# Kernel tuning notes

Measured on AMD Instinct MI355X. Metric: run time of the kernel, lower is better.

The kernel has to match this reference:

```python
import jax, jax.numpy as jnp
import numpy as np

B = 1024          # batch
IN_FEATURES = 20000
N_GROUP = 64
G_IN = 512        # indices gathered per group
H1 = 256          # first Linear out dim per group
GROUP_SIZE = 128  # second Linear out dim per group


def setup_inputs() -> dict:
    key = jax.random.key(0)
    k_x, k_idx, k_w1, k_b1, k_w2, k_b2 = jax.random.split(key, 6)
    x = jax.random.normal(k_x, (B, IN_FEATURES), dtype=jnp.float32)
    idx = jax.random.randint(k_idx, (N_GROUP, G_IN), 0, IN_FEATURES, dtype=jnp.int64)
    # Stacked per-group Linear weights (uniform group shapes allow batching).
    s1 = 1.0 / np.sqrt(G_IN)
    s2 = 1.0 / np.sqrt(H1)
    W1 = jax.random.uniform(k_w1, (N_GROUP, G_IN, H1), jnp.float32, -s1, s1)
    b1 = jax.random.uniform(k_b1, (N_GROUP, H1), jnp.float32, -s1, s1)
    W2 = jax.random.uniform(k_w2, (N_GROUP, H1, GROUP_SIZE), jnp.float32, -s2, s2)
    b2 = jax.random.uniform(k_b2, (N_GROUP, GROUP_SIZE), jnp.float32, -s2, s2)
    return {"x": x, "idx": idx, "W1": W1, "b1": b1, "W2": W2, "b2": b2}


def reference(x, idx, W1, b1, W2, b2):
    # Per-group gather of input columns: [B, n_group, G_IN]
    g = x[:, idx]
    # Two bare Linears per group (no activation, matching the source Sequential).
    h = jnp.einsum('bgi,gio->bgo', g, W1) + b1          # [B, n_group, H1]
    o = jnp.einsum('bgh,gho->bgo', h, W2) + b2          # [B, n_group, GROUP_SIZE]
    # Concat groups along feature dim -> [B, n_group*GROUP_SIZE]
    return o.reshape(o.shape[0], -1)
```

## Files before the change

kernel.cpp:

```cpp
#include <hip/hip_runtime.h>
#include <hip/hip_bf16.h>
#include <stdint.h>


typedef __attribute__((ext_vector_type(4))) float f32x4;
typedef __attribute__((ext_vector_type(8))) __bf16 bf16x8;
typedef __attribute__((ext_vector_type(8))) uint16_t u16x8;

__device__ __forceinline__ uint16_t f2bf(float f) {
    uint32_t u = __float_as_uint(f);
    u += 0x7FFFu + ((u >> 16) & 1u);
    return (uint16_t)(u >> 16);
}

__device__ __forceinline__ uint64_t pack4bf(f32x4 v) {
    return (uint64_t)f2bf(v[0]) | ((uint64_t)f2bf(v[1]) << 16)
         | ((uint64_t)f2bf(v[2]) << 32) | ((uint64_t)f2bf(v[3]) << 48);
}

__device__ __forceinline__ uint32_t bf16lo(float f) {
    uint32_t q;
    asm("v_cvt_pk_bf16_f32 %0, %1, 0" : "=v"(q) : "v"(f));
    return q;
}

__global__ __launch_bounds__(1024, 8) void k_prep(const float* __restrict__ x,
                                                  const int* __restrict__ idx,
                                                  const float* __restrict__ W1,
                                                  const float* __restrict__ b1,
                                                  const float* __restrict__ W2,
                                                  const float* __restrict__ b2,
                                                  uint16_t* __restrict__ Wc,
                                                  float* __restrict__ bias2,
                                                  uint32_t* __restrict__ G32) {
    __shared__ __align__(16) uint8_t smem[81920];
    const int bid = blockIdx.x;
    const int t = threadIdx.x;

    if (bid < 256) {
        uint16_t* As = (uint16_t*)smem;
        uint16_t* Bs = As + 5120;
        const int g = bid >> 2, mt = bid & 3;
        const int wid = t >> 6, l = t & 63;
        const int wm = wid >> 2, wn = wid & 3;
        const int q = l >> 4, lm = l & 15;
        const float* W1g = W1 + ((size_t)g * 512 + (size_t)mt * 128) * 256;
        const float* W2g = W2 + (size_t)g * 256 * 128;
        f32x4 acc[2][2];
        #pragma unroll
        for (int mi = 0; mi < 2; ++mi)
            #pragma unroll
            for (int ni = 0; ni < 2; ++ni) {
                f32x4 z = {0.f, 0.f, 0.f, 0.f};
                acc[mi][ni] = z;
            }
        for (int kt = 0; kt < 8; ++kt) {
            __syncthreads();
            {
                int m = t >> 3, c4 = t & 7;
                f32x4 v = *(const f32x4*)(W1g + (size_t)m * 256 + kt * 32 + c4 * 4);
                *(uint64_t*)&As[m * 40 + c4 * 4] = pack4bf(v);
            }
            {
                int h = t >> 5, n4 = t & 31;
                f32x4 v = *(const f32x4*)(W2g + (size_t)(kt * 32 + h) * 128 + n4 * 4);
                *(uint64_t*)&Bs[h * 132 + n4 * 4] = pack4bf(v);
            }
            __syncthreads();
            bf16x8 a[2];
            #pragma unroll
            for (int mi = 0; mi < 2; ++mi)
                a[mi] = *(const bf16x8*)&As[(wm * 32 + mi * 16 + lm) * 40 + q * 8];
            #pragma unroll
            for (int ni = 0; ni < 2; ++ni) {
                int n = wn * 32 + ni * 16 + lm;
                u16x8 bu;
                #pragma unroll
                for (int j = 0; j < 8; ++j) bu[j] = Bs[(q * 8 + j) * 132 + n];
                bf16x8 bv = __builtin_bit_cast(bf16x8, bu);
                #pragma unroll
                for (int mi = 0; mi < 2; ++mi)
                    acc[mi][ni] = __builtin_amdgcn_mfma_f32_16x16x32_bf16(a[mi], bv, acc[mi][ni], 0, 0, 0);
            }
        }
        uint16_t* Wcg = Wc + (size_t)g * 128 * 512;
        #pragma unroll
        for (int mi = 0; mi < 2; ++mi) {
            int k0 = mt * 128 + wm * 32 + mi * 16 + q * 4;
            #pragma unroll
            for (int ni = 0; ni < 2; ++ni) {
                int n = wn * 32 + ni * 16 + lm;
                *(uint64_t*)&Wcg[(size_t)n * 512 + k0] = pack4bf(acc[mi][ni]);
            }
        }
    } else if (bid < 320) {
        if (t < 128) {
            const int g = bid - 256, n = t;
            const float* w = W2 + (size_t)g * 256 * 128 + n;
            const float* bb = b1 + g * 256;
            float s = b2[g * 128 + n];
            for (int h = 0; h < 256; ++h) s += bb[h] * w[(size_t)h * 128];
            bias2[g * 128 + n] = s;
        }
    } else {
        uint32_t* sh32 = (uint32_t*)smem;
        const int gb = bid - 320;
        const int b0 = gb * 2, b1r = b0 + 1;
        const float* xr0 = x + (size_t)b0 * 20000;
        const float* xr1 = xr0 + 20000;

        f32x4 r0[5], r1[5];
        #pragma unroll
        for (int i = 0; i < 5; ++i) {
            int c = t + i * 1024;
            int cs = c < 5000 ? c : 4999;
            r0[i] = *(const f32x4*)(xr0 + (size_t)cs * 4);
        }
        #pragma unroll
        for (int i = 0; i < 5; ++i) {
            int c = t + i * 1024;
            int cs = c < 5000 ? c : 4999;
            r1[i] = *(const f32x4*)(xr1 + (size_t)cs * 4);
        }
        #pragma unroll
        for (int i = 0; i < 5; ++i) {
            int c = t + i * 1024;
            uint4 qv;
            qv.x = bf16lo(r0[i][0]);
            qv.y = bf16lo(r0[i][1]);
            qv.z = bf16lo(r0[i][2]);
            qv.w = bf16lo(r0[i][3]);
            *(uint4*)&sh32[c * 4] = qv;
        }
        #pragma unroll
        for (int i = 0; i < 5; ++i) {
            int c = t + i * 1024;
            uint16_t* hp = (uint16_t*)&sh32[c * 4];
            #pragma unroll
            for (int j = 0; j < 4; ++j)
                hp[j * 2 + 1] = (uint16_t)bf16lo(r1[i][j]);
        }
        __syncthreads();

        const int4* idx4 = (const int4*)idx;
        uint32_t* rowA = G32 + (size_t)b0 * 16384;
        uint32_t* rowB = G32 + (size_t)b1r * 16384;
        #pragma unroll
        for (int it = 0; it < 4; ++it) {
            int j8 = t + it * 1024;
            int4 va = idx4[j8 * 2];
            int4 vb = idx4[j8 * 2 + 1];
            uint32_t f0 = sh32[va.x], f1 = sh32[va.y];
            uint32_t f2 = sh32[va.z], f3 = sh32[va.w];
            uint32_t f4 = sh32[vb.x], f5 = sh32[vb.y];
            uint32_t f6 = sh32[vb.z], f7 = sh32[vb.w];
            uint4 p0, p1;
            p0.x = __builtin_amdgcn_perm(f1, f0, 0x05040100u);
            p0.y = __builtin_amdgcn_perm(f3, f2, 0x05040100u);
            p0.z = __builtin_amdgcn_perm(f5, f4, 0x05040100u);
            p0.w = __builtin_amdgcn_perm(f7, f6, 0x05040100u);
            p1.x = __builtin_amdgcn_perm(f1, f0, 0x07060302u);
            p1.y = __builtin_amdgcn_perm(f3, f2, 0x07060302u);
            p1.z = __builtin_amdgcn_perm(f5, f4, 0x07060302u);
            p1.w = __builtin_amdgcn_perm(f7, f6, 0x07060302u);
            *(uint4*)&rowA[j8 * 4] = p0;
            *(uint4*)&rowB[j8 * 4] = p1;
        }
    }
}

__global__ __launch_bounds__(256) void k_gemm(const uint16_t* __restrict__ G,
                                              const uint16_t* __restrict__ Wc,
                                              const float* __restrict__ bias2,
                                              float* __restrict__ out) {
    __shared__ uint16_t sh[12288];
    uint16_t* As = sh;
    uint16_t* Bs = sh + 4096;
    const int wg = (blockIdx.x & 7) * 128 + (blockIdx.x >> 3);
    const int g = wg >> 4, mt = wg & 15;
    const int t = threadIdx.x;
    const int wid = t >> 6, l = t & 63;
    const int wm = wid >> 1, wn = wid & 1;
    const int q = l >> 4, lm = l & 15;
    const int lrow = l >> 3;
    const int lcolsw = ((l & 7) ^ lrow) * 8;
    const uint16_t* Ga = G + (size_t)mt * 64 * 32768 + (size_t)g * 512;
    const uint16_t* Wa = Wc + (size_t)g * 65536;

    f32x4 acc[2][4];
    #pragma unroll
    for (int mi = 0; mi < 2; ++mi)
        #pragma unroll
        for (int ni = 0; ni < 4; ++ni) {
            f32x4 z = {0.f, 0.f, 0.f, 0.f};
            acc[mi][ni] = z;
        }

    for (int kt = 0; kt < 8; ++kt) {
        __syncthreads();
        #pragma unroll
        for (int i = 0; i < 2; ++i) {
            const int rowbase = wid * 8 + i * 32;
            const uint16_t* sA = Ga + (size_t)(rowbase + lrow) * 32768 + kt * 64 + lcolsw;
            __builtin_amdgcn_global_load_lds(
                (const __attribute__((address_space(1))) void*)sA,
                (__attribute__((address_space(3))) void*)(As + rowbase * 64), 16, 0, 0);
        }
        #pragma unroll
        for (int i = 0; i < 4; ++i) {
            const int rowbase = wid * 8 + i * 32;
            const uint16_t* sB = Wa + (size_t)(rowbase + lrow) * 512 + kt * 64 + lcolsw;
            __builtin_amdgcn_global_load_lds(
                (const __attribute__((address_space(1))) void*)sB,
                (__attribute__((address_space(3))) void*)(Bs + rowbase * 64), 16, 0, 0);
        }
        __syncthreads();
        #pragma unroll
        for (int kk = 0; kk < 2; ++kk) {
            bf16x8 a[2], b[4];
            #pragma unroll
            for (int mi = 0; mi < 2; ++mi) {
                int row = wm * 32 + mi * 16 + lm;
                int off = row * 64 + ((kk * 32 + q * 8) ^ ((lm & 7) * 8));
                a[mi] = *(const bf16x8*)&As[off];
            }
            #pragma unroll
            for (int ni = 0; ni < 4; ++ni) {
                int row = wn * 64 + ni * 16 + lm;
                int off = row * 64 + ((kk * 32 + q * 8) ^ ((lm & 7) * 8));
                b[ni] = *(const bf16x8*)&Bs[off];
            }
            #pragma unroll
            for (int mi = 0; mi < 2; ++mi)
                #pragma unroll
                for (int ni = 0; ni < 4; ++ni)
                    acc[mi][ni] = __builtin_amdgcn_mfma_f32_16x16x32_bf16(a[mi], b[ni], acc[mi][ni], 0, 0, 0);
        }
    }
    float bn[4];
    #pragma unroll
    for (int ni = 0; ni < 4; ++ni) bn[ni] = bias2[g * 128 + wn * 64 + ni * 16 + lm];
    #pragma unroll
    for (int mi = 0; mi < 2; ++mi)
        #pragma unroll
        for (int ni = 0; ni < 4; ++ni) {
            int col = g * 128 + wn * 64 + ni * 16 + lm;
            #pragma unroll
            for (int r = 0; r < 4; ++r) {
                int brow = mt * 64 + wm * 32 + mi * 16 + q * 4 + r;
                out[(size_t)brow * 8192 + col] = acc[mi][ni][r] + bn[ni];
            }
        }
}

extern "C" void kernel_launch(void* const* d_in, const int* in_sizes, int n_in,
                              void* d_out, int out_size, void* d_ws, size_t ws_size,
                              hipStream_t stream) {
    (void)in_sizes; (void)n_in; (void)out_size; (void)ws_size;
    const float* x   = (const float*)d_in[0];
    const int*   idx = (const int*)d_in[1];
    const float* W1  = (const float*)d_in[2];
    const float* b1  = (const float*)d_in[3];
    const float* W2  = (const float*)d_in[4];
    const float* b2  = (const float*)d_in[5];
    float* out = (float*)d_out;

    uint16_t* G     = (uint16_t*)d_ws;
    uint16_t* Wc    = (uint16_t*)((char*)d_ws + (size_t)(64 << 20));
    float*    bias2 = (float*)   ((char*)d_ws + (size_t)(72 << 20));

    k_prep<<<832, 1024, 0, stream>>>(x, idx, W1, b1, W2, b2, Wc, bias2, (uint32_t*)G);
    k_gemm<<<1024, 256, 0, stream>>>(G, Wc, bias2, out);
}
```

Baseline: 57.60 us.

## Split gather blocks into two staged rows with separate bf16 buffers

Gather blocks used to load two x rows, interleave them as packed bf16 pairs in one LDS array, and emit both output rows with permute ops. Now each row is staged alone into its own 16-bit LDS buffer using a paired bf16 convert, then gathered, so the second row's loads can overlap the first row's gather. Row order alternates with block parity, which may spread memory traffic. In exchange the gather now does 16-bit LDS reads and shift/or packing, there are two barriers, and fewer registers hold loaded data at once.

```diff
diff --git a/kernel.cpp b/kernel.cpp
--- a/kernel.cpp
+++ b/kernel.cpp
@@ -18,10 +18,41 @@
          | ((uint64_t)f2bf(v[2]) << 32) | ((uint64_t)f2bf(v[3]) << 48);
 }
 
-__device__ __forceinline__ uint32_t bf16lo(float f) {
-    uint32_t q;
-    asm("v_cvt_pk_bf16_f32 %0, %1, 0" : "=v"(q) : "v"(f));
-    return q;
+__device__ __forceinline__ void stage_row(uint16_t* buf, const float* __restrict__ xrow,
+                                          int t) {
+    #pragma unroll
+    for (int i = 0; i < 5; ++i) {
+        int c = t + i * 1024;
+        int cs = c < 5000 ? c : 4999;
+        f32x4 v = *(const f32x4*)(xrow + (size_t)cs * 4);
+        uint32_t lo, hi;
+        asm("v_cvt_pk_bf16_f32 %0, %1, %2" : "=v"(lo) : "v"(v[0]), "v"(v[1]));
+        asm("v_cvt_pk_bf16_f32 %0, %1, %2" : "=v"(hi) : "v"(v[2]), "v"(v[3]));
+        uint2 p2; p2.x = lo; p2.y = hi;
+        *(uint2*)&buf[c * 4] = p2;
+    }
+}
+
+__device__ __forceinline__ void gather_row(const uint16_t* buf, const int* __restrict__ idx,
+                                           int t, int b, uint32_t* __restrict__ G32) {
+    const int4* idx4 = (const int4*)idx;
+    uint32_t* row = G32 + (size_t)b * 16384;
+    #pragma unroll
+    for (int it = 0; it < 4; ++it) {
+        int j8 = t + it * 1024;
+        int4 va = idx4[j8 * 2];
+        int4 vb = idx4[j8 * 2 + 1];
+        uint32_t f0 = buf[va.x], f1 = buf[va.y];
+        uint32_t f2 = buf[va.z], f3 = buf[va.w];
+        uint32_t f4 = buf[vb.x], f5 = buf[vb.y];
+        uint32_t f6 = buf[vb.z], f7 = buf[vb.w];
+        uint4 p;
+        p.x = f0 | (f1 << 16);
+        p.y = f2 | (f3 << 16);
+        p.z = f4 | (f5 << 16);
+        p.w = f6 | (f7 << 16);
+        *(uint4*)&row[j8 * 4] = p;
+    }
 }
 
 __global__ __launch_bounds__(1024, 8) void k_prep(const float* __restrict__ x,
@@ -103,69 +134,19 @@
             bias2[g * 128 + n] = s;
         }
     } else {
-        uint32_t* sh32 = (uint32_t*)smem;
+        uint16_t* buf0 = (uint16_t*)smem;
+        uint16_t* buf1 = buf0 + 20480;
         const int gb = bid - 320;
-        const int b0 = gb * 2, b1r = b0 + 1;
-        const float* xr0 = x + (size_t)b0 * 20000;
-        const float* xr1 = xr0 + 20000;
-
-        f32x4 r0[5], r1[5];
-        #pragma unroll
-        for (int i = 0; i < 5; ++i) {
-            int c = t + i * 1024;
-            int cs = c < 5000 ? c : 4999;
-            r0[i] = *(const f32x4*)(xr0 + (size_t)cs * 4);
-        }
-        #pragma unroll
-        for (int i = 0; i < 5; ++i) {
-            int c = t + i * 1024;
-            int cs = c < 5000 ? c : 4999;
-            r1[i] = *(const f32x4*)(xr1 + (size_t)cs * 4);
-        }
-        #pragma unroll
-        for (int i = 0; i < 5; ++i) {
-            int c = t + i * 1024;
-            uint4 qv;
-            qv.x = bf16lo(r0[i][0]);
-            qv.y = bf16lo(r0[i][1]);
-            qv.z = bf16lo(r0[i][2]);
-            qv.w = bf16lo(r0[i][3]);
-            *(uint4*)&sh32[c * 4] = qv;
-        }
-        #pragma unroll
-        for (int i = 0; i < 5; ++i) {
-            int c = t + i * 1024;
-            uint16_t* hp = (uint16_t*)&sh32[c * 4];
-            #pragma unroll
-            for (int j = 0; j < 4; ++j)
-                hp[j * 2 + 1] = (uint16_t)bf16lo(r1[i][j]);
-        }
-        __syncthreads();
-
-        const int4* idx4 = (const int4*)idx;
-        uint32_t* rowA = G32 + (size_t)b0 * 16384;
-        uint32_t* rowB = G32 + (size_t)b1r * 16384;
-        #pragma unroll
-        for (int it = 0; it < 4; ++it) {
-            int j8 = t + it * 1024;
-            int4 va = idx4[j8 * 2];
-            int4 vb = idx4[j8 * 2 + 1];
-            uint32_t f0 = sh32[va.x], f1 = sh32[va.y];
-            uint32_t f2 = sh32[va.z], f3 = sh32[va.w];
-            uint32_t f4 = sh32[vb.x], f5 = sh32[vb.y];
-            uint32_t f6 = sh32[vb.z], f7 = sh32[vb.w];
-            uint4 p0, p1;
-            p0.x = __builtin_amdgcn_perm(f1, f0, 0x05040100u);
-            p0.y = __builtin_amdgcn_perm(f3, f2, 0x05040100u);
-            p0.z = __builtin_amdgcn_perm(f5, f4, 0x05040100u);
-            p0.w = __builtin_amdgcn_perm(f7, f6, 0x05040100u);
-            p1.x = __builtin_amdgcn_perm(f1, f0, 0x07060302u);
-            p1.y = __builtin_amdgcn_perm(f3, f2, 0x07060302u);
-            p1.z = __builtin_amdgcn_perm(f5, f4, 0x07060302u);
-            p1.w = __builtin_amdgcn_perm(f7, f6, 0x07060302u);
-            *(uint4*)&rowA[j8 * 4] = p0;
-            *(uint4*)&rowB[j8 * 4] = p1;
-        }
+        const int par = gb & 1;
+        const int rA = gb * 2 + par;
+        const int rB = gb * 2 + (par ^ 1);
+
+        stage_row(buf0, x + (size_t)rA * 20000, t);
+        __syncthreads();
+        gather_row(buf0, idx, t, rA, G32);
+        stage_row(buf1, x + (size_t)rB * 20000, t);
+        __syncthreads();
+        gather_row(buf1, idx, t, rB, G32);
     }
 }
 
```

New measurement: 58.84 us. +2.2%, slower.
